# Performance work log

Hardware: AMD Instinct MI355X
Metric: run time of the kernel (lower is better)

The kernel has to match this reference:

```python
import jax, jax.numpy as jnp
import numpy as np

N_NODES = 50000
N_EDGES = 800000
IN_DIM = 128
HID = 96
ATTN_HID = 32
OUT_DIM = 16
N_SPOTS = 5000
EPS = 1e-5


def _glorot(k, shape):
    fan_in, fan_out = shape
    lim = float(np.sqrt(6.0 / (fan_in + fan_out)))
    return jax.random.uniform(k, shape, minval=-lim, maxval=lim, dtype=jnp.float32)


def setup_inputs() -> dict:
    key = jax.random.key(0)
    ks = jax.random.split(key, 16)
    f32 = jnp.float32
    inp = {
        'x': jax.random.normal(ks[0], (N_NODES, IN_DIM), dtype=f32),
        'edge_index': jax.random.randint(ks[1], (2, N_EDGES), 0, N_NODES, dtype=jnp.int32),
        'cell_to_spot': jax.random.randint(ks[2], (N_NODES,), 0, N_SPOTS, dtype=jnp.int32),
        'num_spots': N_SPOTS,
        # proj: Linear(IN_DIM, HID) + GraphNorm(HID)
        'proj_W': _glorot(ks[3], (IN_DIM, HID)), 'proj_b': jnp.zeros((HID,), f32),
        'gn0_w': jnp.ones((HID,), f32), 'gn0_b': jnp.zeros((HID,), f32), 'gn0_a': jnp.ones((HID,), f32),
        # GCN layer 1 + GraphNorm
        'gcn1_W': _glorot(ks[4], (HID, HID)), 'gcn1_b': jnp.zeros((HID,), f32),
        'gn1_w': jnp.ones((HID,), f32), 'gn1_b': jnp.zeros((HID,), f32), 'gn1_a': jnp.ones((HID,), f32),
        # GCN layer 2 + GraphNorm
        'gcn2_W': _glorot(ks[5], (HID, HID)), 'gcn2_b': jnp.zeros((HID,), f32),
        'gn2_w': jnp.ones((HID,), f32), 'gn2_b': jnp.zeros((HID,), f32), 'gn2_a': jnp.ones((HID,), f32),
        # spot attention aggregator MLP
        'attn_W1': _glorot(ks[6], (HID, ATTN_HID)), 'attn_b1': jnp.zeros((ATTN_HID,), f32),
        'attn_W2': _glorot(ks[7], (ATTN_HID, 1)), 'attn_b2': jnp.zeros((1,), f32),
        # MLP head: Linear + GraphNorm + ReLU + Linear
        'mlp_W1': _glorot(ks[8], (HID, HID)), 'mlp_b1': jnp.zeros((HID,), f32),
        'mlp_gn_w': jnp.ones((HID,), f32), 'mlp_gn_b': jnp.zeros((HID,), f32), 'mlp_gn_a': jnp.ones((HID,), f32),
        'mlp_W2': _glorot(ks[9], (HID, OUT_DIM)), 'mlp_b2': jnp.zeros((OUT_DIM,), f32),
    }
    return inp


def graph_norm(x, w, b, a):
    # PyG GraphNorm over the single graph (all nodes)
    mean = jnp.mean(x, axis=0, keepdims=True)           # [1, d]
    centered = x - a * mean                              # [n, d]
    var = jnp.mean(centered * centered, axis=0, keepdims=True)
    return w * centered * jax.lax.rsqrt(var + EPS) + b


def gcn_conv(x, W, b, src, dst, n):
    # PyG GCNConv: add self-loops, symmetric normalization
    h = x @ W                                            # [n, d_out]
    deg = jax.ops.segment_sum(jnp.ones((src.shape[0],), x.dtype), dst, num_segments=n) + 1.0
    dinv = jax.lax.rsqrt(deg)                            # deg >= 1 due to self loops
    norm = dinv[src] * dinv[dst]                         # [E]
    agg = jax.ops.segment_sum(h[src] * norm[:, None], dst, num_segments=n)
    agg = agg + (dinv * dinv)[:, None] * h               # self-loop messages
    return agg + b


def segment_softmax(scores, seg, num_segments):
    smax = jax.ops.segment_max(scores, seg, num_segments=num_segments)
    e = jnp.exp(scores - smax[seg])
    denom = jax.ops.segment_sum(e, seg, num_segments=num_segments)
    return e / denom[seg]


def reference(x, edge_index, cell_to_spot, num_spots,
              proj_W, proj_b, gn0_w, gn0_b, gn0_a,
              gcn1_W, gcn1_b, gn1_w, gn1_b, gn1_a,
              gcn2_W, gcn2_b, gn2_w, gn2_b, gn2_a,
              attn_W1, attn_b1, attn_W2, attn_b2,
              mlp_W1, mlp_b1, mlp_gn_w, mlp_gn_b, mlp_gn_a,
              mlp_W2, mlp_b2):
    n = x.shape[0]
    src, dst = edge_index[0], edge_index[1]
    # proj: Linear + GraphNorm + ReLU
    h = jax.nn.relu(graph_norm(x @ proj_W + proj_b, gn0_w, gn0_b, gn0_a))
    # GCN stack
    h = jax.nn.relu(graph_norm(gcn_conv(h, gcn1_W, gcn1_b, src, dst, n), gn1_w, gn1_b, gn1_a))
    h = jax.nn.relu(graph_norm(gcn_conv(h, gcn2_W, gcn2_b, src, dst, n), gn2_w, gn2_b, gn2_a))
    # spot attention aggregation
    scores = (jax.nn.relu(h @ attn_W1 + attn_b1) @ attn_W2 + attn_b2)[:, 0]  # [n]
    attn = segment_softmax(scores, cell_to_spot, num_spots)                  # [n]
    spot = jax.ops.segment_sum(h * attn[:, None], cell_to_spot, num_segments=num_spots)  # [S, d]
    # MLP head
    z = jax.nn.relu(graph_norm(spot @ mlp_W1 + mlp_b1, mlp_gn_w, mlp_gn_b, mlp_gn_a))
    return z @ mlp_W2 + mlp_b2
```

## Files before the change

### kernel.cpp

```cpp
#include <hip/hip_runtime.h>

#define N_NODES 50000
#define N_EDGES 800000
#define IN_DIM 128
#define HID 96
#define ATTN_HID 32
#define OUT_DIM 16
#define N_SPOTS 5000
#define GN_EPS 1e-5f

#define SCAN_NB ((N_NODES + 255) / 256)
#define SCAN_SB ((N_SPOTS + 255) / 256)
#define NXCD 8
#define NRANGE (N_NODES / NXCD)
#define SRANGE (N_SPOTS / NXCD)
#define CSB 256
#define GTHB 6250

typedef short bf16x8 __attribute__((ext_vector_type(8)));
typedef float f32x4 __attribute__((ext_vector_type(4)));

__device__ __align__(16) float g_bufA[N_NODES * HID];
__device__ __align__(16) float g_bufB[N_NODES * HID];
__device__ __align__(16) float g_bufC[N_NODES * HID];
__device__ __align__(16) float g_spot[N_SPOTS * HID];
__device__ float    g_dinv[N_NODES];
__device__ float    g_scores[N_NODES];
__device__ int      g_deg[N_NODES];
__device__ int      g_degs[N_SPOTS];
__device__ int      g_rp[N_NODES + 1];
__device__ int      g_cur[N_NODES];
__device__ int      g_rps[N_SPOTS + 1];
__device__ int      g_curs[N_SPOTS];
__device__ int      g_csrc[N_EDGES];
__device__ int      g_cnode[N_NODES];
__device__ int      g_partN[SCAN_NB];
__device__ int      g_partS[SCAN_SB];
__device__ float    g_gpart[GTHB][2 * HID];
__device__ float    g_Spart[CSB][2 * HID];
__device__ float    g_ab[4 * 2 * HID];

__device__ __forceinline__ float* pick(int id) {
  switch (id) {
    case 0:  return g_bufA;
    case 1:  return g_bufB;
    case 2:  return g_bufC;
    default: return g_spot;
  }
}

__device__ __forceinline__ unsigned short bf16_rn(float f) {
  unsigned u = __float_as_uint(f);
  unsigned r = u + 0x7FFFu + ((u >> 16) & 1u);
  return (unsigned short)(r >> 16);
}

__global__ __launch_bounds__(256) void k_init() {
  int i = blockIdx.x * 256 + threadIdx.x;
  if (i < N_NODES) g_deg[i] = 0;
  if (i < N_SPOTS) g_degs[i] = 0;
}

__global__ __launch_bounds__(256) void k_hist(const int* __restrict__ dst,
                                              const int* __restrict__ c2s) {
  int r = blockIdx.x & 7;
  int cb = blockIdx.x >> 3;
  int stride = (gridDim.x >> 3) * 256;
  int nlo = r * NRANGE, nhi = nlo + NRANGE;
  int slo = r * SRANGE, shi = slo + SRANGE;
  for (int i = cb * 256 + threadIdx.x; i < N_EDGES; i += stride) {
    int d = dst[i];
    if (d >= nlo && d < nhi) atomicAdd(&g_deg[d], 1);
  }
  for (int i = cb * 256 + threadIdx.x; i < N_NODES; i += stride) {
    int sp = c2s[i];
    if (sp >= slo && sp < shi) atomicAdd(&g_degs[sp], 1);
  }
}

__global__ __launch_bounds__(256) void k_scan1() {
  bool isS = blockIdx.x >= SCAN_NB;
  int b = isS ? blockIdx.x - SCAN_NB : blockIdx.x;
  const int n = isS ? N_SPOTS : N_NODES;
  const int* deg = isS ? g_degs : g_deg;
  int i = b * 256 + threadIdx.x;
  int v = (i < n) ? deg[i] : 0;
#pragma unroll
  for (int o = 32; o >= 1; o >>= 1) v += __shfl_xor(v, o);
  __shared__ int red[4];
  if ((threadIdx.x & 63) == 0) red[threadIdx.x >> 6] = v;
  __syncthreads();
  if (threadIdx.x == 0)
    (isS ? g_partS : g_partN)[b] = red[0] + red[1] + red[2] + red[3];
}

__global__ __launch_bounds__(256) void k_scan2() {
  bool isS = blockIdx.x == 1;
  int cnt = isS ? SCAN_SB : SCAN_NB;
  int* part = isS ? g_partS : g_partN;
  __shared__ int tmp[256];
  int t = threadIdx.x;
  int v = (t < cnt) ? part[t] : 0;
  tmp[t] = v;
  __syncthreads();
  for (int o = 1; o < 256; o <<= 1) {
    int u = (t >= o) ? tmp[t - o] : 0;
    __syncthreads();
    tmp[t] += u;
    __syncthreads();
  }
  if (t < cnt) part[t] = tmp[t] - v;
}

__global__ __launch_bounds__(256) void k_scan3() {
  bool isS = blockIdx.x >= SCAN_NB;
  int b = isS ? blockIdx.x - SCAN_NB : blockIdx.x;
  const int n = isS ? N_SPOTS : N_NODES;
  const int* deg = isS ? g_degs : g_deg;
  int* rp  = isS ? g_rps  : g_rp;
  int* cur = isS ? g_curs : g_cur;
  const int* part = isS ? g_partS : g_partN;
  __shared__ int tmp[256];
  int t = threadIdx.x;
  int i = b * 256 + t;
  int v = (i < n) ? deg[i] : 0;
  tmp[t] = v;
  __syncthreads();
  for (int o = 1; o < 256; o <<= 1) {
    int u = (t >= o) ? tmp[t - o] : 0;
    __syncthreads();
    tmp[t] += u;
    __syncthreads();
  }
  if (i < n) {
    int off = part[b] + tmp[t] - v;
    rp[i] = off;
    cur[i] = off;
    if (i == n - 1) rp[n] = off + v;
    if (!isS) g_dinv[i] = rsqrtf((float)(v + 1));
  }
}

__global__ __launch_bounds__(256) void k_fill(const int* __restrict__ src,
                                              const int* __restrict__ dst,
                                              const int* __restrict__ c2s) {
  int r = blockIdx.x & 7;
  int cb = blockIdx.x >> 3;
  int stride = (gridDim.x >> 3) * 256;
  int nlo = r * NRANGE, nhi = nlo + NRANGE;
  int slo = r * SRANGE, shi = slo + SRANGE;
  for (int i = cb * 256 + threadIdx.x; i < N_EDGES; i += stride) {
    int d = dst[i];
    if (d >= nlo && d < nhi) {
      int p = atomicAdd(&g_cur[d], 1);
      g_csrc[p] = src[i];
    }
  }
  for (int i = cb * 256 + threadIdx.x; i < N_NODES; i += stride) {
    int sp = c2s[i];
    if (sp >= slo && sp < shi) {
      int p = atomicAdd(&g_curs[sp], 1);
      g_cnode[p] = i;
    }
  }
}

template <int K, bool AFF, bool SCALE>
__global__ __launch_bounds__(256) void k_mfma(const float* __restrict__ Aext,
                                              int a_id, int out_id,
                                              const float* __restrict__ W,
                                              const float* __restrict__ bias,
                                              int stage, int nrows) {
  constexpr int CH = K / 32;
  __shared__ unsigned short WF[CH][6][64][8];
  __shared__ unsigned short WL[CH][6][64][8];
  __shared__ float abs_[2 * HID];
  __shared__ float bs[HID];
  const float* A = Aext ? Aext : pick(a_id);
  float* out = pick(out_id);
  int tid = threadIdx.x;
  if (AFF && tid < 2 * HID) abs_[tid] = g_ab[stage * 2 * HID + tid];
  if (tid < HID) bs[tid] = bias ? bias[tid] : 0.f;
  for (int idx = tid; idx < CH * 6 * 64; idx += 256) {
    int lane = idx & 63;
    int ct = (idx >> 6) % 6;
    int ch = idx / (6 * 64);
    int kbase = ch * 32 + (lane >> 4) * 8;
    int c = ct * 16 + (lane & 15);
#pragma unroll
    for (int j = 0; j < 8; ++j) {
      float w = W[(size_t)(kbase + j) * HID + c];
      unsigned short h = bf16_rn(w);
      WF[ch][ct][lane][j] = h;
      WL[ch][ct][lane][j] = bf16_rn(w - __uint_as_float((unsigned)h << 16));
    }
  }
  __syncthreads();

  int wv = tid >> 6, lane = tid & 63;
  int r0 = blockIdx.x * 64 + wv * 16;
  int arow = r0 + (lane & 15);
  f32x4 acc[6];
#pragma unroll
  for (int t = 0; t < 6; ++t) acc[t] = (f32x4){0.f, 0.f, 0.f, 0.f};

  for (int ch = 0; ch < CH; ++ch) {
    int ks = ch * 32 + (lane >> 4) * 8;
    float av[8];
    if (arow < nrows) {
      const float4* ap = reinterpret_cast<const float4*>(A + (size_t)arow * K + ks);
      float4 v0 = ap[0], v1 = ap[1];
      av[0] = v0.x; av[1] = v0.y; av[2] = v0.z; av[3] = v0.w;
      av[4] = v1.x; av[5] = v1.y; av[6] = v1.z; av[7] = v1.w;
    } else {
#pragma unroll
      for (int j = 0; j < 8; ++j) av[j] = 0.f;
    }
    if (AFF) {
#pragma unroll
      for (int j = 0; j < 8; ++j)
        av[j] = fmaxf(av[j] * abs_[ks + j] + abs_[HID + ks + j], 0.f);
    }
    bf16x8 ah, al;
#pragma unroll
    for (int j = 0; j < 8; ++j) {
      unsigned short h = bf16_rn(av[j]);
      ah[j] = (short)h;
      al[j] = (short)bf16_rn(av[j] - __uint_as_float((unsigned)h << 16));
    }
#pragma unroll
    for (int ct = 0; ct < 6; ++ct) {
      bf16x8 bh = *reinterpret_cast<const bf16x8*>(&WF[ch][ct][lane][0]);
      bf16x8 bl = *reinterpret_cast<const bf16x8*>(&WL[ch][ct][lane][0]);
      acc[ct] = __builtin_amdgcn_mfma_f32_16x16x32_bf16(al, bh, acc[ct], 0, 0, 0);
      acc[ct] = __builtin_amdgcn_mfma_f32_16x16x32_bf16(ah, bl, acc[ct], 0, 0, 0);
      acc[ct] = __builtin_amdgcn_mfma_f32_16x16x32_bf16(ah, bh, acc[ct], 0, 0, 0);
    }
  }
  int rbase = r0 + (lane >> 4) * 4;
  float dv[4];
#pragma unroll
  for (int j = 0; j < 4; ++j) {
    int r = rbase + j;
    dv[j] = SCALE ? ((r < nrows) ? g_dinv[r] : 0.f) : 1.f;
  }
#pragma unroll
  for (int ct = 0; ct < 6; ++ct) {
    int col = ct * 16 + (lane & 15);
    float bb = bs[col];
#pragma unroll
    for (int j = 0; j < 4; ++j) {
      int r = rbase + j;
      if (r < nrows) out[(size_t)r * HID + col] = acc[ct][j] * dv[j] + bb;
    }
  }
}

template <int K, bool AFF, bool SCALE>
__global__ __launch_bounds__(256) void k_gemm96(const float* __restrict__ Aext,
                                                int a_id, int out_id,
                                                const float* __restrict__ W,
                                                const float* __restrict__ bias,
                                                int stage, int nrows) {
  constexpr int KC = 32;
  constexpr int ROWS = 64;
  __shared__ __align__(16) float Ws[KC][HID];
  __shared__ float xs[ROWS][KC + 1];
  __shared__ float abs_[2 * HID];
  const float* A = Aext ? Aext : pick(a_id);
  float* out = pick(out_id);
  int tid = threadIdx.x;
  if (AFF && tid < 2 * HID) abs_[tid] = g_ab[stage * 2 * HID + tid];
  int r0 = blockIdx.x * ROWS;
  int rg = tid >> 3;
  int cg = (tid & 7) * 12;
  float acc[2][12];
#pragma unroll
  for (int i = 0; i < 2; ++i)
#pragma unroll
    for (int c = 0; c < 12; ++c) acc[i][c] = 0.f;

  for (int k0 = 0; k0 < K; k0 += KC) {
    __syncthreads();
    for (int f = tid; f < KC * HID / 4; f += 256) {
      reinterpret_cast<float4*>(&Ws[0][0])[f] =
          reinterpret_cast<const float4*>(W + (size_t)k0 * HID)[f];
    }
    for (int f = tid; f < ROWS * KC / 4; f += 256) {
      int r = f >> 3;
      int kk = (f & 7) << 2;
      int row = r0 + r;
      float4 v = make_float4(0.f, 0.f, 0.f, 0.f);
      if (row < nrows)
        v = *reinterpret_cast<const float4*>(A + (size_t)row * K + k0 + kk);
      if (AFF) {
        int c = k0 + kk;
        v.x = fmaxf(v.x * abs_[c]     + abs_[HID + c],     0.f);
        v.y = fmaxf(v.y * abs_[c + 1] + abs_[HID + c + 1], 0.f);
        v.z = fmaxf(v.z * abs_[c + 2] + abs_[HID + c + 2], 0.f);
        v.w = fmaxf(v.w * abs_[c + 3] + abs_[HID + c + 3], 0.f);
      }
      xs[r][kk] = v.x; xs[r][kk + 1] = v.y; xs[r][kk + 2] = v.z; xs[r][kk + 3] = v.w;
    }
    __syncthreads();
#pragma unroll
    for (int k = 0; k < KC; ++k) {
      float x0 = xs[rg][k];
      float x1 = xs[rg + 32][k];
#pragma unroll
      for (int c = 0; c < 12; ++c) {
        float wv = Ws[k][cg + c];
        acc[0][c] += x0 * wv;
        acc[1][c] += x1 * wv;
      }
    }
  }
#pragma unroll
  for (int i = 0; i < 2; ++i) {
    int row = r0 + rg + 32 * i;
    if (row < nrows) {
      float sc = SCALE ? g_dinv[row] : 1.f;
#pragma unroll
      for (int c = 0; c < 12; ++c) {
        float v = acc[i][c] * sc;
        if (bias) v += bias[cg + c];
        out[(size_t)row * HID + cg + c] = v;
      }
    }
  }
}

__global__ __launch_bounds__(256) void k_gather(int t_id, const float* __restrict__ b,
                                                int agg_id) {
  const float* __restrict__ t = pick(t_id);
  float* __restrict__ agg = pick(agg_id);
  int g = (blockIdx.x * 256 + threadIdx.x) >> 5;
  int lane = threadIdx.x & 31;
  int beg = g_rp[g], end = g_rp[g + 1];
  const float* __restrict__ tg = t + (size_t)g * HID;
  float a0 = tg[lane], a1 = tg[32 + lane], a2 = tg[64 + lane];
  int e = beg;
  for (; e + 8 <= end; e += 8) {
    const float* p0 = t + (size_t)g_csrc[e]     * HID;
    const float* p1 = t + (size_t)g_csrc[e + 1] * HID;
    const float* p2 = t + (size_t)g_csrc[e + 2] * HID;
    const float* p3 = t + (size_t)g_csrc[e + 3] * HID;
    const float* p4 = t + (size_t)g_csrc[e + 4] * HID;
    const float* p5 = t + (size_t)g_csrc[e + 5] * HID;
    const float* p6 = t + (size_t)g_csrc[e + 6] * HID;
    const float* p7 = t + (size_t)g_csrc[e + 7] * HID;
    a0 += p0[lane]; a1 += p0[32 + lane]; a2 += p0[64 + lane];
    a0 += p1[lane]; a1 += p1[32 + lane]; a2 += p1[64 + lane];
    a0 += p2[lane]; a1 += p2[32 + lane]; a2 += p2[64 + lane];
    a0 += p3[lane]; a1 += p3[32 + lane]; a2 += p3[64 + lane];
    a0 += p4[lane]; a1 += p4[32 + lane]; a2 += p4[64 + lane];
    a0 += p5[lane]; a1 += p5[32 + lane]; a2 += p5[64 + lane];
    a0 += p6[lane]; a1 += p6[32 + lane]; a2 += p6[64 + lane];
    a0 += p7[lane]; a1 += p7[32 + lane]; a2 += p7[64 + lane];
  }
  for (; e < end; ++e) {
    const float* __restrict__ ts = t + (size_t)g_csrc[e] * HID;
    a0 += ts[lane]; a1 += ts[32 + lane]; a2 += ts[64 + lane];
  }
  float di = g_dinv[g];
  float v0 = di * a0 + b[lane];
  float v1 = di * a1 + b[32 + lane];
  float v2 = di * a2 + b[64 + lane];
  size_t o = (size_t)g * HID;
  agg[o + lane]      = v0;
  agg[o + 32 + lane] = v1;
  agg[o + 64 + lane] = v2;
  float q0 = v0, q1 = v1, q2 = v2;
  float r0s = v0 * v0, r1s = v1 * v1, r2s = v2 * v2;
  q0 += __shfl_xor(q0, 32); r0s += __shfl_xor(r0s, 32);
  q1 += __shfl_xor(q1, 32); r1s += __shfl_xor(r1s, 32);
  q2 += __shfl_xor(q2, 32); r2s += __shfl_xor(r2s, 32);
  __shared__ float sred[4][32][6];
  int wv = threadIdx.x >> 6, ln = threadIdx.x & 63;
  if (ln < 32) {
    sred[wv][ln][0] = q0;  sred[wv][ln][1] = r0s;
    sred[wv][ln][2] = q1;  sred[wv][ln][3] = r1s;
    sred[wv][ln][4] = q2;  sred[wv][ln][5] = r2s;
  }
  __syncthreads();
  if (threadIdx.x < 192) {
    int l2 = threadIdx.x / 6, j = threadIdx.x % 6;
    float s = sred[0][l2][j] + sred[1][l2][j] + sred[2][l2][j] + sred[3][l2][j];
    int dim = l2 + (j >> 1) * 32;
    g_gpart[blockIdx.x][(j & 1) ? HID + dim : dim] = s;
  }
}

__global__ __launch_bounds__(256) void k_colred(int count) {
  int tid = threadIdx.x;
  if (tid >= 2 * HID) return;
  float s = 0.f;
  for (int k = blockIdx.x; k < count; k += gridDim.x) s += g_gpart[k][tid];
  g_Spart[blockIdx.x][tid] = s;
}

__global__ __launch_bounds__(256) void k_colstats(int x_id, int nrows) {
  const float4* __restrict__ x4 = reinterpret_cast<const float4*>(pick(x_id));
  int tid = threadIdx.x;
  bool active = tid < 240;
  int c4 = tid % 24, rs = tid / 24;
  float s1[4] = {0.f, 0.f, 0.f, 0.f}, s2[4] = {0.f, 0.f, 0.f, 0.f};
  if (active) {
    for (int r = blockIdx.x * 10 + rs; r < nrows; r += gridDim.x * 10) {
      float4 v = x4[(size_t)r * 24 + c4];
      s1[0] += v.x; s2[0] += v.x * v.x;
      s1[1] += v.y; s2[1] += v.y * v.y;
      s1[2] += v.z; s2[2] += v.z * v.z;
      s1[3] += v.w; s2[3] += v.w * v.w;
    }
  }
  __shared__ float lds1[10][HID], lds2[10][HID];
  if (active) {
#pragma unroll
    for (int j = 0; j < 4; ++j) {
      lds1[rs][c4 * 4 + j] = s1[j];
      lds2[rs][c4 * 4 + j] = s2[j];
    }
  }
  __syncthreads();
  if (tid < 2 * HID) {
    float s = 0.f;
    if (tid < HID) {
#pragma unroll
      for (int k = 0; k < 10; ++k) s += lds1[k][tid];
    } else {
#pragma unroll
      for (int k = 0; k < 10; ++k) s += lds2[k][tid - HID];
    }
    g_Spart[blockIdx.x][tid] = s;
  }
}

__global__ __launch_bounds__(256) void k_gnreduce(int stage,
                                                  const float* __restrict__ w,
                                                  const float* __restrict__ b,
                                                  const float* __restrict__ a,
                                                  float invn) {
  __shared__ float S[2 * HID];
  int tid = threadIdx.x;
  if (tid < 2 * HID) {
    float s0 = 0.f, s1 = 0.f, s2 = 0.f, s3 = 0.f;
    for (int k = 0; k < CSB; k += 4) {
      s0 += g_Spart[k][tid];
      s1 += g_Spart[k + 1][tid];
      s2 += g_Spart[k + 2][tid];
      s3 += g_Spart[k + 3][tid];
    }
    S[tid] = (s0 + s1) + (s2 + s3);
  }
  __syncthreads();
  if (tid < HID) {
    float mean = S[tid] * invn;
    float var = S[HID + tid] * invn + mean * mean * (a[tid] * a[tid] - 2.f * a[tid]);
    float r = rsqrtf(var + GN_EPS);
    float alpha = w[tid] * r;
    float* ab = g_ab + stage * 2 * HID;
    ab[tid] = alpha;
    ab[HID + tid] = b[tid] - alpha * a[tid] * mean;
  }
}

__global__ __launch_bounds__(256) void k_scores(int h_id, int stage,
                                                const float* __restrict__ W1,
                                                const float* __restrict__ b1,
                                                const float* __restrict__ W2,
                                                const float* __restrict__ b2) {
  __shared__ float W1s[HID * ATTN_HID];
  __shared__ float b1s[ATTN_HID], W2s[ATTN_HID];
  __shared__ float abs_[2 * HID];
  const float* h = pick(h_id);
  const float* ab = g_ab + stage * 2 * HID;
  int tid = threadIdx.x;
  for (int f = tid; f < HID * ATTN_HID; f += 256) W1s[f] = W1[f];
  if (tid < ATTN_HID) { b1s[tid] = b1[tid]; W2s[tid] = W2[tid]; }
  if (tid < 2 * HID) abs_[tid] = ab[tid];
  __syncthreads();
  int i = blockIdx.x * 256 + tid;
  if (i >= N_NODES) return;
  float acc[ATTN_HID];
#pragma unroll
  for (int k = 0; k < ATTN_HID; ++k) acc[k] = 0.f;
  const float4* h4 = reinterpret_cast<const float4*>(h + (size_t)i * HID);
  for (int j4 = 0; j4 < HID / 4; ++j4) {
    float4 hv4 = h4[j4];
    int j = j4 * 4;
    float h0 = fmaxf(hv4.x * abs_[j]     + abs_[HID + j],     0.f);
    float h1 = fmaxf(hv4.y * abs_[j + 1] + abs_[HID + j + 1], 0.f);
    float h2 = fmaxf(hv4.z * abs_[j + 2] + abs_[HID + j + 2], 0.f);
    float h3 = fmaxf(hv4.w * abs_[j + 3] + abs_[HID + j + 3], 0.f);
#pragma unroll
    for (int k = 0; k < ATTN_HID; ++k) {
      acc[k] += h0 * W1s[j * ATTN_HID + k] + h1 * W1s[(j + 1) * ATTN_HID + k] +
                h2 * W1s[(j + 2) * ATTN_HID + k] + h3 * W1s[(j + 3) * ATTN_HID + k];
    }
  }
  float s = b2[0];
#pragma unroll
  for (int k = 0; k < ATTN_HID; ++k) s += fmaxf(acc[k] + b1s[k], 0.f) * W2s[k];
  g_scores[i] = s;
}

__global__ __launch_bounds__(256) void k_spotagg(int h_id, int stage) {
  const float* __restrict__ h = pick(h_id);
  const float* ab = g_ab + stage * 2 * HID;
  int g = (blockIdx.x * 256 + threadIdx.x) >> 5;
  int lane = threadIdx.x & 31;
  if (g >= N_SPOTS) return;
  int beg = g_rps[g], end = g_rps[g + 1];
  float m = -1e30f;
  for (int i = beg + lane; i < end; i += 32) m = fmaxf(m, g_scores[g_cnode[i]]);
#pragma unroll
  for (int o = 16; o >= 1; o >>= 1) m = fmaxf(m, __shfl_xor(m, o, 32));
  float al0 = ab[lane],      be0 = ab[HID + lane];
  float al1 = ab[32 + lane], be1 = ab[HID + 32 + lane];
  float al2 = ab[64 + lane], be2 = ab[HID + 64 + lane];
  float a0 = 0.f, a1 = 0.f, a2 = 0.f, denom = 0.f;
  for (int i = beg; i < end; ++i) {
    int nd = g_cnode[i];
    float e = __expf(g_scores[nd] - m);
    denom += e;
    const float* __restrict__ hr = h + (size_t)nd * HID;
    a0 += e * fmaxf(hr[lane] * al0 + be0, 0.f);
    a1 += e * fmaxf(hr[32 + lane] * al1 + be1, 0.f);
    a2 += e * fmaxf(hr[64 + lane] * al2 + be2, 0.f);
  }
  float inv = (denom > 0.f) ? 1.f / denom : 0.f;
  g_spot[g * HID + lane]      = a0 * inv;
  g_spot[g * HID + 32 + lane] = a1 * inv;
  g_spot[g * HID + 64 + lane] = a2 * inv;
}

__global__ __launch_bounds__(256) void k_final(int t3_id, int stage,
                                               const float* __restrict__ W2,
                                               const float* __restrict__ b2,
                                               float* __restrict__ out) {
  __shared__ float W2s[HID * OUT_DIM];
  const float* t3 = pick(t3_id);
  const float* ab = g_ab + stage * 2 * HID;
  int tid = threadIdx.x;
  for (int f = tid; f < HID * OUT_DIM; f += 256) W2s[f] = W2[f];
  __syncthreads();
  int r = blockIdx.x * 16 + (tid >> 4);
  int c = tid & 15;
  if (r >= N_SPOTS) return;
  float acc = b2[c];
  for (int j = 0; j < HID; ++j) {
    float z = fmaxf(t3[(size_t)r * HID + j] * ab[j] + ab[HID + j], 0.f);
    acc += z * W2s[j * OUT_DIM + c];
  }
  out[r * OUT_DIM + c] = acc;
}

extern "C" void kernel_launch(void* const* d_in, const int* in_sizes, int n_in,
                              void* d_out, int out_size, void* d_ws, size_t ws_size,
                              hipStream_t stream) {
  const float* x       = (const float*)d_in[0];
  const int*   ei      = (const int*)d_in[1];
  const int*   src     = ei;
  const int*   dst     = ei + N_EDGES;
  const int*   c2s     = (const int*)d_in[2];
  const float* proj_W  = (const float*)d_in[4];
  const float* proj_b  = (const float*)d_in[5];
  const float* gn0_w   = (const float*)d_in[6];
  const float* gn0_b   = (const float*)d_in[7];
  const float* gn0_a   = (const float*)d_in[8];
  const float* gcn1_W  = (const float*)d_in[9];
  const float* gcn1_b  = (const float*)d_in[10];
  const float* gn1_w   = (const float*)d_in[11];
  const float* gn1_b   = (const float*)d_in[12];
  const float* gn1_a   = (const float*)d_in[13];
  const float* gcn2_W  = (const float*)d_in[14];
  const float* gcn2_b  = (const float*)d_in[15];
  const float* gn2_w   = (const float*)d_in[16];
  const float* gn2_b   = (const float*)d_in[17];
  const float* gn2_a   = (const float*)d_in[18];
  const float* attn_W1 = (const float*)d_in[19];
  const float* attn_b1 = (const float*)d_in[20];
  const float* attn_W2 = (const float*)d_in[21];
  const float* attn_b2 = (const float*)d_in[22];
  const float* mlp_W1  = (const float*)d_in[23];
  const float* mlp_b1  = (const float*)d_in[24];
  const float* mlp_gn_w = (const float*)d_in[25];
  const float* mlp_gn_b = (const float*)d_in[26];
  const float* mlp_gn_a = (const float*)d_in[27];
  const float* mlp_W2  = (const float*)d_in[28];
  const float* mlp_b2  = (const float*)d_in[29];
  float* out = (float*)d_out;

  const float invN = 1.f / (float)N_NODES;
  const float invS = 1.f / (float)N_SPOTS;
  const int GB_N = (N_NODES + 63) / 64;
  const int GB_S = (N_SPOTS + 63) / 64;
  const int XB   = NXCD * 96;
  const int SPB  = (N_SPOTS * 32 + 255) / 256;
  const int SCB  = SCAN_NB + SCAN_SB;

  k_init<<<(N_NODES + 255) / 256, 256, 0, stream>>>();
  k_hist<<<XB, 256, 0, stream>>>(dst, c2s);
  k_scan1<<<SCB, 256, 0, stream>>>();
  k_scan2<<<2, 256, 0, stream>>>();
  k_scan3<<<SCB, 256, 0, stream>>>();
  k_fill<<<XB, 256, 0, stream>>>(src, dst, c2s);

  k_mfma<IN_DIM, false, false><<<GB_N, 256, 0, stream>>>(x, -1, 0, proj_W, proj_b, 0, N_NODES);
  k_colstats<<<CSB, 256, 0, stream>>>(0, N_NODES);
  k_gnreduce<<<1, 256, 0, stream>>>(0, gn0_w, gn0_b, gn0_a, invN);

  k_mfma<HID, true, true><<<GB_N, 256, 0, stream>>>(nullptr, 0, 1, gcn1_W, nullptr, 0, N_NODES);
  k_gather<<<GTHB, 256, 0, stream>>>(1, gcn1_b, 0);
  k_colred<<<CSB, 256, 0, stream>>>(GTHB);
  k_gnreduce<<<1, 256, 0, stream>>>(1, gn1_w, gn1_b, gn1_a, invN);

  k_mfma<HID, true, true><<<GB_N, 256, 0, stream>>>(nullptr, 0, 2, gcn2_W, nullptr, 1, N_NODES);
  k_gather<<<GTHB, 256, 0, stream>>>(2, gcn2_b, 1);
  k_colred<<<CSB, 256, 0, stream>>>(GTHB);
  k_gnreduce<<<1, 256, 0, stream>>>(2, gn2_w, gn2_b, gn2_a, invN);

  k_scores<<<(N_NODES + 255) / 256, 256, 0, stream>>>(1, 2, attn_W1, attn_b1, attn_W2, attn_b2);
  k_spotagg<<<SPB, 256, 0, stream>>>(1, 2);

  k_gemm96<HID, false, false><<<GB_S, 256, 0, stream>>>(nullptr, 3, 2, mlp_W1, mlp_b1, 0, N_SPOTS);
  k_colstats<<<CSB, 256, 0, stream>>>(2, N_SPOTS);
  k_gnreduce<<<1, 256, 0, stream>>>(3, mlp_gn_w, mlp_gn_b, mlp_gn_a, invS);
  k_final<<<(N_SPOTS + 15) / 16, 256, 0, stream>>>(2, 3, mlp_W2, mlp_b2, out);
}
```

Baseline: 366.9 us.

## Fuse GraphNorm stats into GEMM epilogues and collapse reduction kernels with tickets

Column sum and sum-of-squares for GraphNorm are now computed in the MFMA and gemm96 epilogues, which removes the separate colstats pass that re-read the full activation matrix. The colred and gnreduce kernels are merged into one statred kernel that uses a last-block atomic ticket, and scan2 is folded into scan1 the same way. The bf16 hi/lo split of the weights is precomputed once in k_init and read from global memory, replacing the per-block LDS conversion. Fewer launches and less memory traffic come at the cost of threadfence-based cross-block synchronisation, and MFMA B-operands are now read from global or L2 instead of LDS.

```diff
diff --git a/kernel.cpp b/kernel.cpp
--- a/kernel.cpp
+++ b/kernel.cpp
@@ -14,8 +14,9 @@
 #define NXCD 8
 #define NRANGE (N_NODES / NXCD)
 #define SRANGE (N_SPOTS / NXCD)
-#define CSB 256
 #define GTHB 6250
+#define MFB  ((N_NODES + 63) / 64)
+#define STG  128
 
 typedef short bf16x8 __attribute__((ext_vector_type(8)));
 typedef float f32x4 __attribute__((ext_vector_type(4)));
@@ -37,8 +38,11 @@
 __device__ int      g_partN[SCAN_NB];
 __device__ int      g_partS[SCAN_SB];
 __device__ float    g_gpart[GTHB][2 * HID];
-__device__ float    g_Spart[CSB][2 * HID];
+__device__ float    g_Spart[STG][2 * HID];
 __device__ float    g_ab[4 * 2 * HID];
+__device__ int      g_ticket[8];
+__device__ __align__(16) unsigned short g_wf[3][4 * 6 * 64 * 8];
+__device__ __align__(16) unsigned short g_wl[3][4 * 6 * 64 * 8];
 
 __device__ __forceinline__ float* pick(int id) {
   switch (id) {
@@ -55,10 +59,33 @@
   return (unsigned short)(r >> 16);
 }
 
-__global__ __launch_bounds__(256) void k_init() {
+__global__ __launch_bounds__(256) void k_init(const float* __restrict__ pW,
+                                              const float* __restrict__ w1,
+                                              const float* __restrict__ w2) {
   int i = blockIdx.x * 256 + threadIdx.x;
   if (i < N_NODES) g_deg[i] = 0;
   if (i < N_SPOTS) g_degs[i] = 0;
+  if (i < 8) g_ticket[i] = 0;
+  int b = blockIdx.x;
+  if (b < 60 && threadIdx.x < 64) {
+    int lane = threadIdx.x;
+    int m, lb;
+    const float* W;
+    if (b < 24)      { m = 0; lb = b;      W = pW; }
+    else if (b < 42) { m = 1; lb = b - 24; W = w1; }
+    else             { m = 2; lb = b - 42; W = w2; }
+    int ch = lb / 6, ct = lb % 6;
+    int kbase = ch * 32 + (lane >> 4) * 8;
+    int c = ct * 16 + (lane & 15);
+    int off = ((ch * 6 + ct) << 9) + (lane << 3);
+#pragma unroll
+    for (int j = 0; j < 8; ++j) {
+      float w = W[(size_t)(kbase + j) * HID + c];
+      unsigned short h = bf16_rn(w);
+      g_wf[m][off + j] = h;
+      g_wl[m][off + j] = bf16_rn(w - __uint_as_float((unsigned)h << 16));
+    }
+  }
 }
 
 __global__ __launch_bounds__(256) void k_hist(const int* __restrict__ dst,
@@ -90,26 +117,44 @@
   __shared__ int red[4];
   if ((threadIdx.x & 63) == 0) red[threadIdx.x >> 6] = v;
   __syncthreads();
+  if (threadIdx.x == 0) {
+    (isS ? g_partS : g_partN)[b] = red[0] + red[1] + red[2] + red[3];
+    __threadfence();
+  }
+  __syncthreads();
+  __shared__ int last;
   if (threadIdx.x == 0)
-    (isS ? g_partS : g_partN)[b] = red[0] + red[1] + red[2] + red[3];
-}
-
-__global__ __launch_bounds__(256) void k_scan2() {
-  bool isS = blockIdx.x == 1;
-  int cnt = isS ? SCAN_SB : SCAN_NB;
-  int* part = isS ? g_partS : g_partN;
+    last = (atomicAdd(&g_ticket[4], 1) == (int)gridDim.x - 1);
+  __syncthreads();
+  if (!last) return;
+  __threadfence();
   __shared__ int tmp[256];
   int t = threadIdx.x;
-  int v = (t < cnt) ? part[t] : 0;
-  tmp[t] = v;
-  __syncthreads();
-  for (int o = 1; o < 256; o <<= 1) {
-    int u = (t >= o) ? tmp[t - o] : 0;
-    __syncthreads();
-    tmp[t] += u;
-    __syncthreads();
-  }
-  if (t < cnt) part[t] = tmp[t] - v;
+  {
+    int val = (t < SCAN_NB) ? g_partN[t] : 0;
+    tmp[t] = val;
+    __syncthreads();
+    for (int o = 1; o < 256; o <<= 1) {
+      int u = (t >= o) ? tmp[t - o] : 0;
+      __syncthreads();
+      tmp[t] += u;
+      __syncthreads();
+    }
+    if (t < SCAN_NB) g_partN[t] = tmp[t] - val;
+    __syncthreads();
+  }
+  {
+    int val = (t < SCAN_SB) ? g_partS[t] : 0;
+    tmp[t] = val;
+    __syncthreads();
+    for (int o = 1; o < 256; o <<= 1) {
+      int u = (t >= o) ? tmp[t - o] : 0;
+      __syncthreads();
+      tmp[t] += u;
+      __syncthreads();
+    }
+    if (t < SCAN_SB) g_partS[t] = tmp[t] - val;
+  }
 }
 
 __global__ __launch_bounds__(256) void k_scan3() {
@@ -165,36 +210,21 @@
   }
 }
 
-template <int K, bool AFF, bool SCALE>
+template <int K, bool AFF, bool SCALE, bool STATS>
 __global__ __launch_bounds__(256) void k_mfma(const float* __restrict__ Aext,
-                                              int a_id, int out_id,
-                                              const float* __restrict__ W,
+                                              int a_id, int out_id, int m,
                                               const float* __restrict__ bias,
                                               int stage, int nrows) {
   constexpr int CH = K / 32;
-  __shared__ unsigned short WF[CH][6][64][8];
-  __shared__ unsigned short WL[CH][6][64][8];
   __shared__ float abs_[2 * HID];
   __shared__ float bs[HID];
   const float* A = Aext ? Aext : pick(a_id);
   float* out = pick(out_id);
+  const unsigned short* __restrict__ wf = g_wf[m];
+  const unsigned short* __restrict__ wl = g_wl[m];
   int tid = threadIdx.x;
   if (AFF && tid < 2 * HID) abs_[tid] = g_ab[stage * 2 * HID + tid];
   if (tid < HID) bs[tid] = bias ? bias[tid] : 0.f;
-  for (int idx = tid; idx < CH * 6 * 64; idx += 256) {
-    int lane = idx & 63;
-    int ct = (idx >> 6) % 6;
-    int ch = idx / (6 * 64);
-    int kbase = ch * 32 + (lane >> 4) * 8;
-    int c = ct * 16 + (lane & 15);
-#pragma unroll
-    for (int j = 0; j < 8; ++j) {
-      float w = W[(size_t)(kbase + j) * HID + c];
-      unsigned short h = bf16_rn(w);
-      WF[ch][ct][lane][j] = h;
-      WL[ch][ct][lane][j] = bf16_rn(w - __uint_as_float((unsigned)h << 16));
-    }
-  }
   __syncthreads();
 
   int wv = tid >> 6, lane = tid & 63;
@@ -230,8 +260,9 @@
     }
 #pragma unroll
     for (int ct = 0; ct < 6; ++ct) {
-      bf16x8 bh = *reinterpret_cast<const bf16x8*>(&WF[ch][ct][lane][0]);
-      bf16x8 bl = *reinterpret_cast<const bf16x8*>(&WL[ch][ct][lane][0]);
+      int off = ((ch * 6 + ct) << 9) + (lane << 3);
+      bf16x8 bh = *reinterpret_cast<const bf16x8*>(wf + off);
+      bf16x8 bl = *reinterpret_cast<const bf16x8*>(wl + off);
       acc[ct] = __builtin_amdgcn_mfma_f32_16x16x32_bf16(al, bh, acc[ct], 0, 0, 0);
       acc[ct] = __builtin_amdgcn_mfma_f32_16x16x32_bf16(ah, bl, acc[ct], 0, 0, 0);
       acc[ct] = __builtin_amdgcn_mfma_f32_16x16x32_bf16(ah, bh, acc[ct], 0, 0, 0);
@@ -244,6 +275,9 @@
     int r = rbase + j;
     dv[j] = SCALE ? ((r < nrows) ? g_dinv[r] : 0.f) : 1.f;
   }
+  float s1[6], s2[6];
+#pragma unroll
+  for (int ct = 0; ct < 6; ++ct) { s1[ct] = 0.f; s2[ct] = 0.f; }
 #pragma unroll
   for (int ct = 0; ct < 6; ++ct) {
     int col = ct * 16 + (lane & 15);
@@ -251,12 +285,44 @@
 #pragma unroll
     for (int j = 0; j < 4; ++j) {
       int r = rbase + j;
-      if (r < nrows) out[(size_t)r * HID + col] = acc[ct][j] * dv[j] + bb;
-    }
-  }
-}
-
-template <int K, bool AFF, bool SCALE>
+      if (r < nrows) {
+        float v = acc[ct][j] * dv[j] + bb;
+        out[(size_t)r * HID + col] = v;
+        if (STATS) { s1[ct] += v; s2[ct] += v * v; }
+      }
+    }
+  }
+  if constexpr (STATS) {
+#pragma unroll
+    for (int o = 16; o <= 32; o <<= 1) {
+#pragma unroll
+      for (int ct = 0; ct < 6; ++ct) {
+        s1[ct] += __shfl_xor(s1[ct], o);
+        s2[ct] += __shfl_xor(s2[ct], o);
+      }
+    }
+    __shared__ float sr1[4][6][16], sr2[4][6][16];
+    if ((lane & 15) == lane) {
+#pragma unroll
+      for (int ct = 0; ct < 6; ++ct) {
+        sr1[wv][ct][lane] = s1[ct];
+        sr2[wv][ct][lane] = s2[ct];
+      }
+    }
+    __syncthreads();
+    if (tid < 2 * HID) {
+      int c = (tid < HID) ? tid : tid - HID;
+      int ct = c >> 4, l = c & 15;
+      float s = 0.f;
+#pragma unroll
+      for (int w = 0; w < 4; ++w)
+        s += (tid < HID) ? sr1[w][ct][l] : sr2[w][ct][l];
+      g_gpart[blockIdx.x][tid] = s;
+    }
+  }
+}
+
+template <int K, bool AFF, bool SCALE, bool STATS>
 __global__ __launch_bounds__(256) void k_gemm96(const float* __restrict__ Aext,
                                                 int a_id, int out_id,
                                                 const float* __restrict__ W,
@@ -315,6 +381,9 @@
       }
     }
   }
+  float s1[12], s2[12];
+#pragma unroll
+  for (int c = 0; c < 12; ++c) { s1[c] = 0.f; s2[c] = 0.f; }
 #pragma unroll
   for (int i = 0; i < 2; ++i) {
     int row = r0 + rg + 32 * i;
@@ -325,7 +394,34 @@
         float v = acc[i][c] * sc;
         if (bias) v += bias[cg + c];
         out[(size_t)row * HID + cg + c] = v;
-      }
+        if (STATS) { s1[c] += v; s2[c] += v * v; }
+      }
+    }
+  }
+  if constexpr (STATS) {
+#pragma unroll
+    for (int off = 8; off <= 32; off <<= 1) {
+#pragma unroll
+      for (int c = 0; c < 12; ++c) {
+        s1[c] += __shfl_xor(s1[c], off);
+        s2[c] += __shfl_xor(s2[c], off);
+      }
+    }
+    __shared__ float sred[4][8][24];
+    int wv = tid >> 6, ln = tid & 63;
+    if (ln < 8) {
+#pragma unroll
+      for (int c = 0; c < 12; ++c) {
+        sred[wv][ln][2 * c] = s1[c];
+        sred[wv][ln][2 * c + 1] = s2[c];
+      }
+    }
+    __syncthreads();
+    if (tid < 192) {
+      int cg2 = tid / 24, j = tid % 24;
+      float s = sred[0][cg2][j] + sred[1][cg2][j] + sred[2][cg2][j] + sred[3][cg2][j];
+      int col = cg2 * 12 + (j >> 1);
+      g_gpart[blockIdx.x][(j & 1) ? HID + col : col] = s;
     }
   }
 }
@@ -391,67 +487,30 @@
   }
 }
 
-__global__ __launch_bounds__(256) void k_colred(int count) {
+__global__ __launch_bounds__(256) void k_statred(int count, int stage,
+                                                 const float* __restrict__ w,
+                                                 const float* __restrict__ b,
+                                                 const float* __restrict__ a,
+                                                 float invn, int slot) {
   int tid = threadIdx.x;
-  if (tid >= 2 * HID) return;
-  float s = 0.f;
-  for (int k = blockIdx.x; k < count; k += gridDim.x) s += g_gpart[k][tid];
-  g_Spart[blockIdx.x][tid] = s;
-}
-
-__global__ __launch_bounds__(256) void k_colstats(int x_id, int nrows) {
-  const float4* __restrict__ x4 = reinterpret_cast<const float4*>(pick(x_id));
-  int tid = threadIdx.x;
-  bool active = tid < 240;
-  int c4 = tid % 24, rs = tid / 24;
-  float s1[4] = {0.f, 0.f, 0.f, 0.f}, s2[4] = {0.f, 0.f, 0.f, 0.f};
-  if (active) {
-    for (int r = blockIdx.x * 10 + rs; r < nrows; r += gridDim.x * 10) {
-      float4 v = x4[(size_t)r * 24 + c4];
-      s1[0] += v.x; s2[0] += v.x * v.x;
-      s1[1] += v.y; s2[1] += v.y * v.y;
-      s1[2] += v.z; s2[2] += v.z * v.z;
-      s1[3] += v.w; s2[3] += v.w * v.w;
-    }
-  }
-  __shared__ float lds1[10][HID], lds2[10][HID];
-  if (active) {
-#pragma unroll
-    for (int j = 0; j < 4; ++j) {
-      lds1[rs][c4 * 4 + j] = s1[j];
-      lds2[rs][c4 * 4 + j] = s2[j];
-    }
-  }
-  __syncthreads();
   if (tid < 2 * HID) {
     float s = 0.f;
-    if (tid < HID) {
-#pragma unroll
-      for (int k = 0; k < 10; ++k) s += lds1[k][tid];
-    } else {
-#pragma unroll
-      for (int k = 0; k < 10; ++k) s += lds2[k][tid - HID];
-    }
+    for (int k = blockIdx.x; k < count; k += gridDim.x) s += g_gpart[k][tid];
     g_Spart[blockIdx.x][tid] = s;
   }
-}
-
-__global__ __launch_bounds__(256) void k_gnreduce(int stage,
-                                                  const float* __restrict__ w,
-                                                  const float* __restrict__ b,
-                                                  const float* __restrict__ a,
-                                                  float invn) {
+  __threadfence();
+  __syncthreads();
+  __shared__ int last;
+  if (tid == 0)
+    last = (atomicAdd(&g_ticket[slot], 1) == (int)gridDim.x - 1);
+  __syncthreads();
+  if (!last) return;
+  __threadfence();
   __shared__ float S[2 * HID];
-  int tid = threadIdx.x;
   if (tid < 2 * HID) {
-    float s0 = 0.f, s1 = 0.f, s2 = 0.f, s3 = 0.f;
-    for (int k = 0; k < CSB; k += 4) {
-      s0 += g_Spart[k][tid];
-      s1 += g_Spart[k + 1][tid];
-      s2 += g_Spart[k + 2][tid];
-      s3 += g_Spart[k + 3][tid];
-    }
-    S[tid] = (s0 + s1) + (s2 + s3);
+    float s = 0.f;
+    for (int k = 0; k < (int)gridDim.x; ++k) s += g_Spart[k][tid];
+    S[tid] = s;
   }
   __syncthreads();
   if (tid < HID) {
@@ -459,9 +518,8 @@
     float var = S[HID + tid] * invn + mean * mean * (a[tid] * a[tid] - 2.f * a[tid]);
     float r = rsqrtf(var + GN_EPS);
     float alpha = w[tid] * r;
-    float* ab = g_ab + stage * 2 * HID;
-    ab[tid] = alpha;
-    ab[HID + tid] = b[tid] - alpha * a[tid] * mean;
+    g_ab[stage * 2 * HID + tid] = alpha;
+    g_ab[stage * 2 * HID + HID + tid] = b[tid] - alpha * a[tid] * mean;
   }
 }
 
@@ -594,38 +652,32 @@
 
   const float invN = 1.f / (float)N_NODES;
   const float invS = 1.f / (float)N_SPOTS;
-  const int GB_N = (N_NODES + 63) / 64;
   const int GB_S = (N_SPOTS + 63) / 64;
   const int XB   = NXCD * 96;
   const int SPB  = (N_SPOTS * 32 + 255) / 256;
   const int SCB  = SCAN_NB + SCAN_SB;
 
-  k_init<<<(N_NODES + 255) / 256, 256, 0, stream>>>();
+  k_init<<<(N_NODES + 255) / 256, 256, 0, stream>>>(proj_W, gcn1_W, gcn2_W);
   k_hist<<<XB, 256, 0, stream>>>(dst, c2s);
   k_scan1<<<SCB, 256, 0, stream>>>();
-  k_scan2<<<2, 256, 0, stream>>>();
   k_scan3<<<SCB, 256, 0, stream>>>();
   k_fill<<<XB, 256, 0, stream>>>(src, dst, c2s);
 
-  k_mfma<IN_DIM, false, false><<<GB_N, 256, 0, stream>>>(x, -1, 0, proj_W, proj_b, 0, N_NODES);
-  k_colstats<<<CSB, 256, 0, stream>>>(0, N_NODES);
-  k_gnreduce<<<1, 256, 0, stream>>>(0, gn0_w, gn0_b, gn0_a, invN);
-
-  k_mfma<HID, true, true><<<GB_N, 256, 0, stream>>>(nullptr, 0, 1, gcn1_W, nullptr, 0, N_NODES);
+  k_mfma<IN_DIM, false, false, true><<<MFB, 256, 0, stream>>>(x, -1, 0, 0, proj_b, 0, N_NODES);
+  k_statred<<<STG, 256, 0, stream>>>(MFB, 0, gn0_w, gn0_b, gn0_a, invN, 0);
+
+  k_mfma<HID, true, true, false><<<MFB, 256, 0, stream>>>(nullptr, 0, 1, 1, nullptr, 0, N_NODES);
   k_gather<<<GTHB, 256, 0, stream>>>(1, gcn1_b, 0);
-  k_colred<<<CSB, 256, 0, stream>>>(GTHB);
-  k_gnreduce<<<1, 256, 0, stream>>>(1, gn1_w, gn1_b, gn1_a, invN);
-
-  k_mfma<HID, true, true><<<GB_N, 256, 0, stream>>>(nullptr, 0, 2, gcn2_W, nullptr, 1, N_NODES);
+  k_statred<<<STG, 256, 0, stream>>>(GTHB, 1, gn1_w, gn1_b, gn1_a, invN, 1);
+
+  k_mfma<HID, true, true, false><<<MFB, 256, 0, stream>>>(nullptr, 0, 2, 2, nullptr, 1, N_NODES);
   k_gather<<<GTHB, 256, 0, stream>>>(2, gcn2_b, 1);
-  k_colred<<<CSB, 256, 0, stream>>>(GTHB);
-  k_gnreduce<<<1, 256, 0, stream>>>(2, gn2_w, gn2_b, gn2_a, invN);
+  k_statred<<<STG, 256, 0, stream>>>(GTHB, 2, gn2_w, gn2_b, gn2_a, invN, 2);
 
   k_scores<<<(N_NODES + 255) / 256, 256, 0, stream>>>(1, 2, attn_W1, attn_b1, attn_W2, attn_b2);
   k_spotagg<<<SPB, 256, 0, stream>>>(1, 2);
 
-  k_gemm96<HID, false, false><<<GB_S, 256, 0, stream>>>(nullptr, 3, 2, mlp_W1, mlp_b1, 0, N_SPOTS);
-  k_colstats<<<CSB, 256, 0, stream>>>(2, N_SPOTS);
-  k_gnreduce<<<1, 256, 0, stream>>>(3, mlp_gn_w, mlp_gn_b, mlp_gn_a, invS);
+  k_gemm96<HID, false, false, true><<<GB_S, 256, 0, stream>>>(nullptr, 3, 2, mlp_W1, mlp_b1, 0, N_SPOTS);
+  k_statred<<<STG, 256, 0, stream>>>(GB_S, 3, mlp_gn_w, mlp_gn_b, mlp_gn_a, invS, 3);
   k_final<<<(N_SPOTS + 15) / 16, 256, 0, stream>>>(2, 3, mlp_W2, mlp_b2, out);
 }
```

New measurement: 511.8 us. 1.4x slower.
